# Kernel tuning notes

Measured on AMD Instinct MI355X. Metric: run time of the kernel, lower is better.

The kernel has to match this reference:

```python
import jax, jax.numpy as jnp
import numpy as np

C_IN, C_OUT = 256, 128

def setup_inputs() -> dict:
    key = jax.random.key(0)
    k1, k2, k3, k4, k5, k6 = jax.random.split(key, 6)
    B, H, W = 8, 64, 64
    p = jax.random.normal(k1, (B, C_IN, H, W), dtype=jnp.float32)
    b = jax.random.normal(k2, (B, C_IN, H, W), dtype=jnp.float32)
    # 1x1 conv weights (Conv2d with kernel 1 == pointwise matmul) + biases
    sq = 1.0 / np.sqrt(C_IN)
    Wq = jax.random.uniform(k3, (C_OUT, C_IN), jnp.float32, -sq, sq)
    bq = jax.random.uniform(k4, (C_OUT,), jnp.float32, -sq, sq)
    Wk = jax.random.uniform(k5, (C_OUT, C_IN), jnp.float32, -sq, sq)
    bk = jax.random.uniform(k6, (C_OUT,), jnp.float32, -sq, sq)
    return {"p": p, "b": b, "Wq": Wq, "bq": bq, "Wk": Wk, "bk": bk}

def reference(p, b, Wq, bq, Wk, bk):
    B, C, H, W = p.shape
    N = H * W
    # 1x1 convs -> flatten spatial dim to N
    q = jnp.einsum('bchw,oc->bhwo', p, Wq) + bq          # [B,H,W,Co]
    q = q.reshape(B, N, -1).astype(jnp.float32)           # [B,N,Co] (query permuted)
    k = jnp.einsum('bchw,oc->bohw', b, Wk) + bk[None, :, None, None]
    k = k.reshape(B, -1, N).astype(jnp.float32)           # [B,Co,N]
    energy = jnp.einsum('bnc,bcm->bnm', q, k)             # [B,N,N] unscaled
    attention = jax.nn.softmax(energy, axis=-1)           # softmax over keys
    value = b.reshape(B, C, N)                            # [B,C,N]
    out = jnp.einsum('bnm,bcm->bcn', attention, value)    # [B,C,N]
    return out.reshape(B, C, H, W)
```

## Files before the change

### kernel.cpp

```cpp
#include <hip/hip_runtime.h>
#include <hip/hip_bf16.h>
#include <math.h>


#define B_   8
#define CIN  256
#define COUT 128
#define NN   4096

typedef _Float16 half8  __attribute__((ext_vector_type(8)));
typedef short    short8 __attribute__((ext_vector_type(8)));
typedef float    f32x4  __attribute__((ext_vector_type(4)));

#define LOG2E 1.44269504088896340736f

__device__ __forceinline__ unsigned short f2h(float f) {
    union { _Float16 h; unsigned short u; } v; v.h = (_Float16)f;
    return v.u;
}
__device__ __forceinline__ unsigned int cvt_pk_bf16(float lo, float hi) {
    unsigned int r;
    asm("v_cvt_pk_bf16_f32 %0, %1, %2" : "=v"(r) : "v"(lo), "v"(hi));
    return r;
}
__device__ __forceinline__ unsigned int pkrtz(float lo, float hi) {
    typedef __fp16 fp16x2 __attribute__((ext_vector_type(2)));
    union { fp16x2 h; unsigned int u; } c;
    c.h = __builtin_amdgcn_cvt_pkrtz(lo, hi);
    return c.u;
}
__device__ __forceinline__ float dpp_xor1(float x) {
    union { float f; int i; } u; u.f = x;
    u.i = __builtin_amdgcn_mov_dpp(u.i, 0xB1, 0xF, 0xF, true);
    return u.f;
}
__device__ __forceinline__ void dma16(void* lds, const void* g) {
    __builtin_amdgcn_global_load_lds(
        (const __attribute__((address_space(1))) unsigned int*)g,
        (__attribute__((address_space(3))) unsigned int*)lds,
        16, 0, 0);
}

__global__ __launch_bounds__(256) void cvt_w(const float* __restrict__ Wq,
                                             const float* __restrict__ Wk,
                                             const float* __restrict__ bq,
                                             _Float16* __restrict__ Whq,
                                             _Float16* __restrict__ Whk,
                                             float* __restrict__ bqs) {
    const int bx = blockIdx.x, t = threadIdx.x;
    const int isK = (bx >= 32);
    const float* src = isK ? Wk : Wq;
    _Float16* dst = isK ? Whk : Whq;
    const float scale = isK ? 1.0f : LOG2E;
    const int idx = (bx & 31) * 256 + t;
    float4 v = ((const float4*)src)[idx];
    unsigned long long pk = (unsigned long long)f2h(v.x * scale)
                          | ((unsigned long long)f2h(v.y * scale) << 16)
                          | ((unsigned long long)f2h(v.z * scale) << 32)
                          | ((unsigned long long)f2h(v.w * scale) << 48);
    ((unsigned long long*)dst)[idx] = pk;
    if (bx == 0 && t < COUT) bqs[t] = bq[t] * LOG2E;
}

__global__ __launch_bounds__(256) void kv_prep(
        const float* __restrict__ Bv,
        const _Float16* __restrict__ Whk,
        const float* __restrict__ bk,
        _Float16* __restrict__ Ktt,
        unsigned short* __restrict__ Vb)
{
    __shared__ __align__(16) unsigned short T[64 * 136];
    const int bx = blockIdx.x;
    const int b  = bx >> 6, n0 = (bx & 63) << 6;
    const int t  = threadIdx.x;

    {
        const int cr = t >> 2;
        const int nch = (t & 3) << 4;
#pragma unroll
        for (int it = 0; it < 4; ++it) {
            const int c = it * 64 + cr;
            const float* src = Bv + ((size_t)(b * CIN + c) * NN + n0 + nch);
            unsigned int o2[8];
#pragma unroll
            for (int k = 0; k < 4; ++k) {
                float4 f = *(const float4*)(src + k * 4);
                o2[k * 2]     = cvt_pk_bf16(f.x, f.y);
                o2[k * 2 + 1] = cvt_pk_bf16(f.z, f.w);
            }
            unsigned short* dst = Vb + (size_t)(b * CIN + c) * NN + n0 + nch;
            *(int4*)dst = *(int4*)&o2[0];
            *(int4*)(dst + 8) = *(int4*)&o2[4];
        }
    }

    const int w = t >> 6, lane = t & 63, l15 = lane & 15, quad = lane >> 4, q8 = quad * 8;

    half8 a[8];
    {
        const float* Xa = Bv + ((size_t)(b * CIN + q8) * NN) + n0 + w * 16 + l15;
#pragma unroll
        for (int s = 0; s < 8; ++s) {
            const float* xs = Xa + (size_t)s * 32 * NN;
            float av[8];
#pragma unroll
            for (int j = 0; j < 8; ++j) av[j] = xs[(size_t)j * NN];
            union { half8 h; unsigned int u[4]; } af;
#pragma unroll
            for (int j = 0; j < 4; ++j) af.u[j] = pkrtz(av[2 * j], av[2 * j + 1]);
            a[s] = af.h;
        }
    }

    f32x4 D[8];
#pragma unroll
    for (int og = 0; og < 8; ++og) D[og] = (f32x4){0.f, 0.f, 0.f, 0.f};
    const _Float16* wbase = Whk + (size_t)l15 * CIN + q8;
#pragma unroll
    for (int s = 0; s < 8; ++s) {
        const _Float16* wp = wbase + s * 32;
#pragma unroll
        for (int og = 0; og < 8; ++og) {
            half8 wfv = *(const half8*)(wp + og * 16 * CIN);
            D[og] = __builtin_amdgcn_mfma_f32_16x16x32_f16(a[s], wfv, D[og], 0, 0, 0);
        }
    }

    const int nrow = w * 16 + quad * 4;
#pragma unroll
    for (int og = 0; og < 8; ++og) {
        const int o = og * 16 + l15;
        const float bo = bk[o];
        const int c = o >> 3, j = o & 7;
        const int sw = (c & 7) << 2;
#pragma unroll
        for (int r2 = 0; r2 < 4; ++r2) {
            const int n = nrow + r2;
            const int tl = n >> 5, m = n & 31;
            T[tl * 4096 + (c * 32 + ((m + sw) & 31)) * 8 + j] = f2h(D[og][r2] + bo);
        }
    }
    __syncthreads();
    _Float16* dstk = Ktt + ((size_t)(b * 128 + (n0 >> 5)) * 4096 + t * 32);
    const unsigned short* srck = T + t * 32;
#pragma unroll
    for (int k = 0; k < 4; ++k)
        ((int4*)dstk)[k] = ((const int4*)srck)[k];
}

__global__ __launch_bounds__(256, 3) void flash_kernel(const float* __restrict__ Pin,
                                                       const _Float16* __restrict__ Whq,
                                                       const float* __restrict__ bqs,
                                                       const _Float16* __restrict__ Ktt,
                                                       const unsigned short* __restrict__ V,
                                                       float* __restrict__ out) {
    __shared__ __align__(16) char SH[27136];
    _Float16*       K0sh = (_Float16*)(SH);
    _Float16*       K1sh = (_Float16*)(SH + 8192);
    unsigned short* P0sh = (unsigned short*)(SH + 16384);
    unsigned short* P1sh = (unsigned short*)(SH + 21504);
    float*          Lsh  = (float*)(SH + 26624);
    unsigned short* T    = (unsigned short*)SH;

    const int bx   = blockIdx.x;
    const int b    = bx >> 6;
    const int q0   = (bx & 63) << 6;
    const int t    = threadIdx.x;
    const int w    = t >> 6;
    const int lane = t & 63;
    const int l15  = lane & 15;
    const int quad = lane >> 4;
    const int q8   = quad * 8;

    const _Float16* Kb = Ktt + (size_t)b * 128 * 4096;
    const unsigned short* Vg = V + (size_t)b * CIN * NN;

    half8 Qf[4];
    {
        half8 a[8];
        const float* Xa = Pin + ((size_t)(b * CIN + q8) * NN) + q0 + w * 16 + l15;
#pragma unroll
        for (int s = 0; s < 8; ++s) {
            const float* xs = Xa + (size_t)s * 32 * NN;
            float av[8];
#pragma unroll
            for (int j = 0; j < 8; ++j) av[j] = xs[(size_t)j * NN];
            union { half8 h; unsigned int u[4]; } af;
#pragma unroll
            for (int j = 0; j < 4; ++j) af.u[j] = pkrtz(av[2 * j], av[2 * j + 1]);
            a[s] = af.h;
        }
        f32x4 D[8];
#pragma unroll
        for (int og = 0; og < 8; ++og) D[og] = (f32x4){0.f, 0.f, 0.f, 0.f};
        const _Float16* wbase = Whq + (size_t)l15 * CIN + q8;
#pragma unroll
        for (int s = 0; s < 8; ++s) {
            const _Float16* wp = wbase + s * 32;
#pragma unroll
            for (int og = 0; og < 8; ++og) {
                half8 wfv = *(const half8*)(wp + og * 16 * CIN);
                D[og] = __builtin_amdgcn_mfma_f32_16x16x32_f16(a[s], wfv, D[og], 0, 0, 0);
            }
        }
        const int nrow = w * 16 + quad * 4;
#pragma unroll
        for (int og = 0; og < 8; ++og) {
            const int o = og * 16 + l15;
            const float bo = bqs[o];
#pragma unroll
            for (int r2 = 0; r2 < 4; ++r2)
                T[(nrow + r2) * 136 + o] = f2h(D[og][r2] + bo);
        }
        __syncthreads();
#pragma unroll
        for (int s = 0; s < 4; ++s)
            Qf[s] = *(const half8*)&T[(w * 16 + l15) * 136 + s * 32 + q8];
        __syncthreads();
    }

    f32x4 O[16];
#pragma unroll
    for (int i = 0; i < 16; ++i) O[i] = (f32x4){0.f, 0.f, 0.f, 0.f};
    float lsum[4] = {0.f, 0.f, 0.f, 0.f};

    const unsigned short* Vlane = Vg + (size_t)(w * 64 + l15) * NN + q8;
    short8 VA[4], VB[4];

    auto issueK = [&](int kt, _Float16* Kd) {
        const _Float16* gk = Kb + (size_t)kt * 4096;
        dma16(Kd + (w * 2 + 0) * 512, gk + (w * 2 + 0) * 512 + lane * 8);
        dma16(Kd + (w * 2 + 1) * 512, gk + (w * 2 + 1) * 512 + lane * 8);
    };
    auto loadV = [&](int kt, short8* Vd) {
#pragma unroll
        for (int cj = 0; cj < 4; ++cj)
            Vd[cj] = *(const short8*)(Vlane + (size_t)cj * 16 * NN + kt * 32);
    };

    auto halfstep = [&](int kt, const _Float16* Kc, _Float16* Kn,
                        unsigned short* Pc, short8* Vcur) {
        if (kt + 1 < 128) issueK(kt + 1, Kn);

        f32x4 S0 = {0.f, 0.f, 0.f, 0.f}, S1 = {0.f, 0.f, 0.f, 0.f};
        __builtin_amdgcn_s_setprio(1);
#pragma unroll
        for (int s = 0; s < 4; ++s) {
            const int kc = 4 * s + quad;
            const int sw = (kc & 7) << 2;
            const int x0 = (l15 + sw) & 31;
            half8 kf0 = *(const half8*)(Kc + (kc * 32 + x0) * 8);
            half8 kf1 = *(const half8*)(Kc + (kc * 32 + (x0 ^ 16)) * 8);
            S0 = __builtin_amdgcn_mfma_f32_16x16x32_f16(Qf[s], kf0, S0, 0, 0, 0);
            S1 = __builtin_amdgcn_mfma_f32_16x16x32_f16(Qf[s], kf1, S1, 0, 0, 0);
        }
        __builtin_amdgcn_s_setprio(0);

        f32x4 E0, E1;
#pragma unroll
        for (int r = 0; r < 4; ++r) {
            E0[r] = exp2f(S0[r]);
            E1[r] = exp2f(S1[r]);
            lsum[r] += E0[r] + E1[r];
        }
        {
            f32x4 P0, P1;
#pragma unroll
            for (int r = 0; r < 4; ++r) { P0[r] = dpp_xor1(E0[r]); P1[r] = dpp_xor1(E1[r]); }
            const int odd = l15 & 1;
            unsigned short* wp0 = Pc + w * 640
                                + (((quad << 2) + (odd << 1)) * 40) + (l15 & ~1);
            unsigned int pk0 = cvt_pk_bf16(odd ? P0[2] : E0[0], odd ? E0[2] : P0[0]);
            unsigned int pk1 = cvt_pk_bf16(odd ? P0[3] : E0[1], odd ? E0[3] : P0[1]);
            unsigned int pk2 = cvt_pk_bf16(odd ? P1[2] : E1[0], odd ? E1[2] : P1[0]);
            unsigned int pk3 = cvt_pk_bf16(odd ? P1[3] : E1[1], odd ? E1[3] : P1[1]);
            *(unsigned int*)&wp0[0]  = pk0;
            *(unsigned int*)&wp0[40] = pk1;
            *(unsigned int*)&wp0[16] = pk2;
            *(unsigned int*)&wp0[56] = pk3;
        }

        __syncthreads();

        {
            short8 pf[4];
#pragma unroll
            for (int ni = 0; ni < 4; ++ni)
                pf[ni] = *(const short8*)(Pc + (ni * 16 + l15) * 40 + q8);
            __builtin_amdgcn_s_setprio(1);
#pragma unroll
            for (int cj = 0; cj < 4; ++cj) {
                short8 vf = Vcur[cj];
#pragma unroll
                for (int ni = 0; ni < 4; ++ni)
                    O[ni * 4 + cj] = __builtin_amdgcn_mfma_f32_16x16x32_bf16(pf[ni], vf, O[ni * 4 + cj], 0, 0, 0);
            }
            __builtin_amdgcn_s_setprio(0);
        }
        if (kt + 2 < 128) loadV(kt + 2, Vcur);
    };

    issueK(0, K0sh);
    loadV(0, VA);
    loadV(1, VB);
    __syncthreads();

#pragma unroll 1
    for (int kt = 0; kt < 128; kt += 2) {
        halfstep(kt,     K0sh, K1sh, P0sh, VA);
        halfstep(kt + 1, K1sh, K0sh, P1sh, VB);
    }

#pragma unroll
    for (int r = 0; r < 4; ++r) {
        float s = lsum[r];
        s += __shfl_xor(s, 1);
        s += __shfl_xor(s, 2);
        s += __shfl_xor(s, 4);
        s += __shfl_xor(s, 8);
        if (l15 == 0) Lsh[w * 16 + (quad << 2) + r] = s;
    }
    __syncthreads();
    float* ob = out + (size_t)b * CIN * NN + q0;
#pragma unroll
    for (int ni = 0; ni < 4; ++ni) {
        const f32x4 lv = *(const f32x4*)&Lsh[ni * 16 + (quad << 2)];
        f32x4 linv;
#pragma unroll
        for (int r = 0; r < 4; ++r) linv[r] = 1.0f / lv[r];
        const int nb = ni * 16 + (quad << 2);
#pragma unroll
        for (int cj = 0; cj < 4; ++cj) {
            const int c = w * 64 + cj * 16 + l15;
            f32x4 val = O[ni * 4 + cj];
#pragma unroll
            for (int r = 0; r < 4; ++r) val[r] *= linv[r];
            *(f32x4*)(ob + (size_t)c * NN + nb) = val;
        }
    }
}

extern "C" void kernel_launch(void* const* d_in, const int* in_sizes, int n_in,
                              void* d_out, int out_size, void* d_ws, size_t ws_size,
                              hipStream_t stream) {
    const float* p  = (const float*)d_in[0];
    const float* bv = (const float*)d_in[1];
    const float* Wq = (const float*)d_in[2];
    const float* bq = (const float*)d_in[3];
    const float* Wk = (const float*)d_in[4];
    const float* bk = (const float*)d_in[5];
    float* outp = (float*)d_out;

    char* ws = (char*)d_ws;
    const size_t szK = (size_t)B_ * NN * COUT * 2;
    const size_t szV = (size_t)B_ * NN * CIN * 2;
    const size_t szW = (size_t)COUT * CIN * 2;
    _Float16*       Ktt = (_Float16*)ws;
    unsigned short* Vb  = (unsigned short*)(ws + szK);
    _Float16*       Whq = (_Float16*)(ws + szK + szV);
    _Float16*       Whk = (_Float16*)(ws + szK + szV + szW);
    float*          bqs = (float*)(ws + szK + szV + 2 * szW);

    cvt_w<<<64, 256, 0, stream>>>(Wq, Wk, bq, Whq, Whk, bqs);
    kv_prep<<<512, 256, 0, stream>>>(bv, Whk, bk, Ktt, Vb);
    flash_kernel<<<512, 256, 0, stream>>>(p, Whq, bqs, Ktt, Vb, outp);
}
```

Before: 274.4 us.

## Process two key tiles per barrier with 4-deep K/P LDS rings; split V conversion

The flash loop now runs the QK/softmax phase for two key tiles, then a single barrier, then both PV phases. The K and P tiles live in 4-slot LDS rings, and K prefetch is issued two tiles ahead. This halves the workgroup barriers per key tile and gives the K DMA more time to land. The bf16 conversion of V moves out of kv_prep into its own flat elementwise kernel. That adds one launch, and LDS per block roughly doubles, which may tighten occupancy at 3 blocks per CU.

```diff
diff --git a/kernel.cpp b/kernel.cpp
--- a/kernel.cpp
+++ b/kernel.cpp
@@ -62,37 +62,32 @@
     if (bx == 0 && t < COUT) bqs[t] = bq[t] * LOG2E;
 }
 
+__global__ __launch_bounds__(256) void vb_conv(const float* __restrict__ Bv,
+                                               unsigned short* __restrict__ Vb) {
+    const size_t i = ((size_t)blockIdx.x * 256 + threadIdx.x) * 16;
+    const float* src = Bv + i;
+    unsigned int o2[8];
+#pragma unroll
+    for (int k = 0; k < 4; ++k) {
+        float4 f = ((const float4*)src)[k];
+        o2[k * 2]     = cvt_pk_bf16(f.x, f.y);
+        o2[k * 2 + 1] = cvt_pk_bf16(f.z, f.w);
+    }
+    unsigned short* dst = Vb + i;
+    *(int4*)dst = *(int4*)&o2[0];
+    *(int4*)(dst + 8) = *(int4*)&o2[4];
+}
+
 __global__ __launch_bounds__(256) void kv_prep(
         const float* __restrict__ Bv,
         const _Float16* __restrict__ Whk,
         const float* __restrict__ bk,
-        _Float16* __restrict__ Ktt,
-        unsigned short* __restrict__ Vb)
+        _Float16* __restrict__ Ktt)
 {
     __shared__ __align__(16) unsigned short T[64 * 136];
     const int bx = blockIdx.x;
     const int b  = bx >> 6, n0 = (bx & 63) << 6;
     const int t  = threadIdx.x;
-
-    {
-        const int cr = t >> 2;
-        const int nch = (t & 3) << 4;
-#pragma unroll
-        for (int it = 0; it < 4; ++it) {
-            const int c = it * 64 + cr;
-            const float* src = Bv + ((size_t)(b * CIN + c) * NN + n0 + nch);
-            unsigned int o2[8];
-#pragma unroll
-            for (int k = 0; k < 4; ++k) {
-                float4 f = *(const float4*)(src + k * 4);
-                o2[k * 2]     = cvt_pk_bf16(f.x, f.y);
-                o2[k * 2 + 1] = cvt_pk_bf16(f.z, f.w);
-            }
-            unsigned short* dst = Vb + (size_t)(b * CIN + c) * NN + n0 + nch;
-            *(int4*)dst = *(int4*)&o2[0];
-            *(int4*)(dst + 8) = *(int4*)&o2[4];
-        }
-    }
 
     const int w = t >> 6, lane = t & 63, l15 = lane & 15, quad = lane >> 4, q8 = quad * 8;
 
@@ -154,13 +149,11 @@
                                                        const _Float16* __restrict__ Ktt,
                                                        const unsigned short* __restrict__ V,
                                                        float* __restrict__ out) {
-    __shared__ __align__(16) char SH[27136];
-    _Float16*       K0sh = (_Float16*)(SH);
-    _Float16*       K1sh = (_Float16*)(SH + 8192);
-    unsigned short* P0sh = (unsigned short*)(SH + 16384);
-    unsigned short* P1sh = (unsigned short*)(SH + 21504);
-    float*          Lsh  = (float*)(SH + 26624);
-    unsigned short* T    = (unsigned short*)SH;
+    __shared__ __align__(16) char SH[53504];
+    _Float16*       Ksh = (_Float16*)(SH);
+    unsigned short* Psh = (unsigned short*)(SH + 32768);
+    float*          Lsh = (float*)(SH + 53248);
+    unsigned short* T   = (unsigned short*)SH;
 
     const int bx   = blockIdx.x;
     const int b    = bx >> 6;
@@ -227,7 +220,8 @@
     const unsigned short* Vlane = Vg + (size_t)(w * 64 + l15) * NN + q8;
     short8 VA[4], VB[4];
 
-    auto issueK = [&](int kt, _Float16* Kd) {
+    auto issueK = [&](int kt) {
+        _Float16* Kd = Ksh + (size_t)(kt & 3) * 4096;
         const _Float16* gk = Kb + (size_t)kt * 4096;
         dma16(Kd + (w * 2 + 0) * 512, gk + (w * 2 + 0) * 512 + lane * 8);
         dma16(Kd + (w * 2 + 1) * 512, gk + (w * 2 + 1) * 512 + lane * 8);
@@ -238,10 +232,9 @@
             Vd[cj] = *(const short8*)(Vlane + (size_t)cj * 16 * NN + kt * 32);
     };
 
-    auto halfstep = [&](int kt, const _Float16* Kc, _Float16* Kn,
-                        unsigned short* Pc, short8* Vcur) {
-        if (kt + 1 < 128) issueK(kt + 1, Kn);
-
+    auto Sphase = [&](int kt) {
+        const _Float16* Kc = Ksh + (size_t)(kt & 3) * 4096;
+        unsigned short* Pc = Psh + (size_t)(kt & 3) * 2560;
         f32x4 S0 = {0.f, 0.f, 0.f, 0.f}, S1 = {0.f, 0.f, 0.f, 0.f};
         __builtin_amdgcn_s_setprio(1);
 #pragma unroll
@@ -263,52 +256,54 @@
             E1[r] = exp2f(S1[r]);
             lsum[r] += E0[r] + E1[r];
         }
-        {
-            f32x4 P0, P1;
-#pragma unroll
-            for (int r = 0; r < 4; ++r) { P0[r] = dpp_xor1(E0[r]); P1[r] = dpp_xor1(E1[r]); }
-            const int odd = l15 & 1;
-            unsigned short* wp0 = Pc + w * 640
-                                + (((quad << 2) + (odd << 1)) * 40) + (l15 & ~1);
-            unsigned int pk0 = cvt_pk_bf16(odd ? P0[2] : E0[0], odd ? E0[2] : P0[0]);
-            unsigned int pk1 = cvt_pk_bf16(odd ? P0[3] : E0[1], odd ? E0[3] : P0[1]);
-            unsigned int pk2 = cvt_pk_bf16(odd ? P1[2] : E1[0], odd ? E1[2] : P1[0]);
-            unsigned int pk3 = cvt_pk_bf16(odd ? P1[3] : E1[1], odd ? E1[3] : P1[1]);
-            *(unsigned int*)&wp0[0]  = pk0;
-            *(unsigned int*)&wp0[40] = pk1;
-            *(unsigned int*)&wp0[16] = pk2;
-            *(unsigned int*)&wp0[56] = pk3;
-        }
-
-        __syncthreads();
-
-        {
-            short8 pf[4];
+        f32x4 P0, P1;
+#pragma unroll
+        for (int r = 0; r < 4; ++r) { P0[r] = dpp_xor1(E0[r]); P1[r] = dpp_xor1(E1[r]); }
+        const int odd = l15 & 1;
+        unsigned short* wp0 = Pc + w * 640
+                            + (((quad << 2) + (odd << 1)) * 40) + (l15 & ~1);
+        unsigned int pk0 = cvt_pk_bf16(odd ? P0[2] : E0[0], odd ? E0[2] : P0[0]);
+        unsigned int pk1 = cvt_pk_bf16(odd ? P0[3] : E0[1], odd ? E0[3] : P0[1]);
+        unsigned int pk2 = cvt_pk_bf16(odd ? P1[2] : E1[0], odd ? E1[2] : P1[0]);
+        unsigned int pk3 = cvt_pk_bf16(odd ? P1[3] : E1[1], odd ? E1[3] : P1[1]);
+        *(unsigned int*)&wp0[0]  = pk0;
+        *(unsigned int*)&wp0[40] = pk1;
+        *(unsigned int*)&wp0[16] = pk2;
+        *(unsigned int*)&wp0[56] = pk3;
+    };
+
+    auto PVphase = [&](int kt, const short8* Vcur) {
+        const unsigned short* Pc = Psh + (size_t)(kt & 3) * 2560;
+        short8 pf[4];
+#pragma unroll
+        for (int ni = 0; ni < 4; ++ni)
+            pf[ni] = *(const short8*)(Pc + (ni * 16 + l15) * 40 + q8);
+        __builtin_amdgcn_s_setprio(1);
+#pragma unroll
+        for (int cj = 0; cj < 4; ++cj) {
+            short8 vf = Vcur[cj];
 #pragma unroll
             for (int ni = 0; ni < 4; ++ni)
-                pf[ni] = *(const short8*)(Pc + (ni * 16 + l15) * 40 + q8);
-            __builtin_amdgcn_s_setprio(1);
-#pragma unroll
-            for (int cj = 0; cj < 4; ++cj) {
-                short8 vf = Vcur[cj];
-#pragma unroll
-                for (int ni = 0; ni < 4; ++ni)
-                    O[ni * 4 + cj] = __builtin_amdgcn_mfma_f32_16x16x32_bf16(pf[ni], vf, O[ni * 4 + cj], 0, 0, 0);
-            }
-            __builtin_amdgcn_s_setprio(0);
-        }
-        if (kt + 2 < 128) loadV(kt + 2, Vcur);
+                O[ni * 4 + cj] = __builtin_amdgcn_mfma_f32_16x16x32_bf16(pf[ni], vf, O[ni * 4 + cj], 0, 0, 0);
+        }
+        __builtin_amdgcn_s_setprio(0);
     };
 
-    issueK(0, K0sh);
-    loadV(0, VA);
-    loadV(1, VB);
+    issueK(0); issueK(1);
+    loadV(0, VA); loadV(1, VB);
     __syncthreads();
 
 #pragma unroll 1
     for (int kt = 0; kt < 128; kt += 2) {
-        halfstep(kt,     K0sh, K1sh, P0sh, VA);
-        halfstep(kt + 1, K1sh, K0sh, P1sh, VB);
+        if (kt + 2 < 128) issueK(kt + 2);
+        if (kt + 3 < 128) issueK(kt + 3);
+        Sphase(kt);
+        Sphase(kt + 1);
+        __syncthreads();
+        PVphase(kt, VA);
+        if (kt + 2 < 128) loadV(kt + 2, VA);
+        PVphase(kt + 1, VB);
+        if (kt + 3 < 128) loadV(kt + 3, VB);
     }
 
 #pragma unroll
@@ -362,6 +357,7 @@
     float*          bqs = (float*)(ws + szK + szV + 2 * szW);
 
     cvt_w<<<64, 256, 0, stream>>>(Wq, Wk, bq, Whq, Whk, bqs);
-    kv_prep<<<512, 256, 0, stream>>>(bv, Whk, bk, Ktt, Vb);
+    vb_conv<<<2048, 256, 0, stream>>>(bv, Vb);
+    kv_prep<<<512, 256, 0, stream>>>(bv, Whk, bk, Ktt);
     flash_kernel<<<512, 256, 0, stream>>>(p, Whq, bqs, Ktt, Vb, outp);
 }
```

After: 292.8 us. +6.7%, slower.

## Deepen V prefetch to four buffers and use partial vmcnt barrier

Applied to the files above, without the earlier changes.

Rotates the value-tile prefetch through four register buffers and issues each load two iterations ahead, before the score phase. The full __syncthreads between the score and PV phases becomes an explicit lgkmcnt(0), a vmcnt(4) wait and a raw s_barrier. This lets the in-flight V loads stay outstanding across the barrier, so the loop only waits for the K DMA. The extra V buffers raise VGPR pressure, and correctness now depends on the hand-counted outstanding-load numbers.

```diff
diff --git a/kernel.cpp b/kernel.cpp
--- a/kernel.cpp
+++ b/kernel.cpp
@@ -225,9 +225,10 @@
     float lsum[4] = {0.f, 0.f, 0.f, 0.f};
 
     const unsigned short* Vlane = Vg + (size_t)(w * 64 + l15) * NN + q8;
-    short8 VA[4], VB[4];
-
-    auto issueK = [&](int kt, _Float16* Kd) {
+    short8 V0[4], V1[4], V2[4], V3[4];
+
+    auto issueK = [&](int kt) {
+        _Float16* Kd = (kt & 1) ? K1sh : K0sh;
         const _Float16* gk = Kb + (size_t)kt * 4096;
         dma16(Kd + (w * 2 + 0) * 512, gk + (w * 2 + 0) * 512 + lane * 8);
         dma16(Kd + (w * 2 + 1) * 512, gk + (w * 2 + 1) * 512 + lane * 8);
@@ -238,10 +239,9 @@
             Vd[cj] = *(const short8*)(Vlane + (size_t)cj * 16 * NN + kt * 32);
     };
 
-    auto halfstep = [&](int kt, const _Float16* Kc, _Float16* Kn,
-                        unsigned short* Pc, short8* Vcur) {
-        if (kt + 1 < 128) issueK(kt + 1, Kn);
-
+    auto Sphase = [&](int kt) {
+        const _Float16* Kc = (kt & 1) ? K1sh : K0sh;
+        unsigned short* Pc = (kt & 1) ? P1sh : P0sh;
         f32x4 S0 = {0.f, 0.f, 0.f, 0.f}, S1 = {0.f, 0.f, 0.f, 0.f};
         __builtin_amdgcn_s_setprio(1);
 #pragma unroll
@@ -263,54 +263,65 @@
             E1[r] = exp2f(S1[r]);
             lsum[r] += E0[r] + E1[r];
         }
-        {
-            f32x4 P0, P1;
-#pragma unroll
-            for (int r = 0; r < 4; ++r) { P0[r] = dpp_xor1(E0[r]); P1[r] = dpp_xor1(E1[r]); }
-            const int odd = l15 & 1;
-            unsigned short* wp0 = Pc + w * 640
-                                + (((quad << 2) + (odd << 1)) * 40) + (l15 & ~1);
-            unsigned int pk0 = cvt_pk_bf16(odd ? P0[2] : E0[0], odd ? E0[2] : P0[0]);
-            unsigned int pk1 = cvt_pk_bf16(odd ? P0[3] : E0[1], odd ? E0[3] : P0[1]);
-            unsigned int pk2 = cvt_pk_bf16(odd ? P1[2] : E1[0], odd ? E1[2] : P1[0]);
-            unsigned int pk3 = cvt_pk_bf16(odd ? P1[3] : E1[1], odd ? E1[3] : P1[1]);
-            *(unsigned int*)&wp0[0]  = pk0;
-            *(unsigned int*)&wp0[40] = pk1;
-            *(unsigned int*)&wp0[16] = pk2;
-            *(unsigned int*)&wp0[56] = pk3;
-        }
-
-        __syncthreads();
-
-        {
-            short8 pf[4];
+        f32x4 P0, P1;
+#pragma unroll
+        for (int r = 0; r < 4; ++r) { P0[r] = dpp_xor1(E0[r]); P1[r] = dpp_xor1(E1[r]); }
+        const int odd = l15 & 1;
+        unsigned short* wp0 = Pc + w * 640
+                            + (((quad << 2) + (odd << 1)) * 40) + (l15 & ~1);
+        unsigned int pk0 = cvt_pk_bf16(odd ? P0[2] : E0[0], odd ? E0[2] : P0[0]);
+        unsigned int pk1 = cvt_pk_bf16(odd ? P0[3] : E0[1], odd ? E0[3] : P0[1]);
+        unsigned int pk2 = cvt_pk_bf16(odd ? P1[2] : E1[0], odd ? E1[2] : P1[0]);
+        unsigned int pk3 = cvt_pk_bf16(odd ? P1[3] : E1[1], odd ? E1[3] : P1[1]);
+        *(unsigned int*)&wp0[0]  = pk0;
+        *(unsigned int*)&wp0[40] = pk1;
+        *(unsigned int*)&wp0[16] = pk2;
+        *(unsigned int*)&wp0[56] = pk3;
+    };
+
+    auto PVphase = [&](int kt, const short8* Vcur) {
+        const unsigned short* Pc = (kt & 1) ? P1sh : P0sh;
+        short8 pf[4];
+#pragma unroll
+        for (int ni = 0; ni < 4; ++ni)
+            pf[ni] = *(const short8*)(Pc + (ni * 16 + l15) * 40 + q8);
+        __builtin_amdgcn_s_setprio(1);
+#pragma unroll
+        for (int cj = 0; cj < 4; ++cj) {
+            short8 vf = Vcur[cj];
 #pragma unroll
             for (int ni = 0; ni < 4; ++ni)
-                pf[ni] = *(const short8*)(Pc + (ni * 16 + l15) * 40 + q8);
-            __builtin_amdgcn_s_setprio(1);
-#pragma unroll
-            for (int cj = 0; cj < 4; ++cj) {
-                short8 vf = Vcur[cj];
-#pragma unroll
-                for (int ni = 0; ni < 4; ++ni)
-                    O[ni * 4 + cj] = __builtin_amdgcn_mfma_f32_16x16x32_bf16(pf[ni], vf, O[ni * 4 + cj], 0, 0, 0);
-            }
-            __builtin_amdgcn_s_setprio(0);
-        }
-        if (kt + 2 < 128) loadV(kt + 2, Vcur);
-    };
-
-    issueK(0, K0sh);
-    loadV(0, VA);
-    loadV(1, VB);
+                O[ni * 4 + cj] = __builtin_amdgcn_mfma_f32_16x16x32_bf16(pf[ni], vf, O[ni * 4 + cj], 0, 0, 0);
+        }
+        __builtin_amdgcn_s_setprio(0);
+    };
+
+    auto quarter = [&](int kt, short8* Vcur, short8* Vld) {
+        if (kt + 1 < 128) issueK(kt + 1);
+        if (kt + 2 < 128) loadV(kt + 2, Vld);
+        Sphase(kt);
+        asm volatile("s_waitcnt lgkmcnt(0)" ::: "memory");
+        asm volatile("s_waitcnt vmcnt(4)" ::: "memory");
+        __builtin_amdgcn_sched_barrier(0);
+        __builtin_amdgcn_s_barrier();
+        __builtin_amdgcn_sched_barrier(0);
+        PVphase(kt, Vcur);
+    };
+
+    issueK(0);
+    loadV(0, V0);
+    loadV(1, V1);
     __syncthreads();
 
 #pragma unroll 1
-    for (int kt = 0; kt < 128; kt += 2) {
-        halfstep(kt,     K0sh, K1sh, P0sh, VA);
-        halfstep(kt + 1, K1sh, K0sh, P1sh, VB);
-    }
-
+    for (int kt = 0; kt < 128; kt += 4) {
+        quarter(kt,     V0, V2);
+        quarter(kt + 1, V1, V3);
+        quarter(kt + 2, V2, V0);
+        quarter(kt + 3, V3, V1);
+    }
+
+    __syncthreads();
 #pragma unroll
     for (int r = 0; r < 4; ++r) {
         float s = lsum[r];
```

Measured after the change: 540.8 us. 1.97x slower.
